# Kernel tuning notes

Hardware: AMD Instinct MI355X
Metric: run time of the kernel (lower is better)

## Reference

```python
import jax, jax.numpy as jnp
import numpy as np

L, D, DB, P, B = 33, 2048, 1024, 24, 2048
EPS = 1e-5

def _ln(x, g, b):
    # LayerNorm over last axis, eps matches torch default 1e-5
    mu = jnp.mean(x, axis=-1, keepdims=True)
    var = jnp.mean(jnp.square(x - mu), axis=-1, keepdims=True)
    return (x - mu) * jax.lax.rsqrt(var + EPS) * g + b

def setup_inputs() -> dict:
    key = jax.random.key(0)
    ks = jax.random.split(key, 8)
    s1 = 1.0 / np.sqrt(D)   # fan-in style scaling to keep activations sane
    s2 = 1.0 / np.sqrt(DB)
    sp = 1.0 / np.sqrt(P)
    return {
        "x":      jax.random.normal(ks[0], (B, L, D), jnp.float32),
        "pos_emb": jax.random.uniform(ks[1], (L, P), jnp.float32),
        "Wk":     jax.random.normal(ks[2], (P, D), jnp.float32) * sp,
        "W1":     jax.random.normal(ks[3], (L, D, DB), jnp.float32) * s1,
        "b1":     jnp.zeros((L, DB), jnp.float32),
        "ln1_g":  jnp.ones((L, DB), jnp.float32),
        "ln1_b":  jnp.zeros((L, DB), jnp.float32),
        "W2":     jax.random.normal(ks[4], (L, DB, D), jnp.float32) * s2,
        "b2":     jnp.zeros((L, D), jnp.float32),
        "ln2_g":  jnp.ones((L, D), jnp.float32),
        "ln2_b":  jnp.zeros((L, D), jnp.float32),
        "Wq1":    jax.random.normal(ks[5], (D, DB), jnp.float32) * s1,
        "bq1":    jnp.zeros((DB,), jnp.float32),
        "lnq_g":  jnp.ones((DB,), jnp.float32),
        "lnq_b":  jnp.zeros((DB,), jnp.float32),
        "Wq2":    jax.random.normal(ks[6], (DB, D), jnp.float32) * s2,
        "bq2":    jnp.zeros((D,), jnp.float32),
    }

def reference(x, pos_emb, Wk, W1, b1, ln1_g, ln1_b, W2, b2, ln2_g, ln2_b,
              Wq1, bq1, lnq_g, lnq_b, Wq2, bq2):
    # x: [B, L, D]
    z_L = x[:, -1, :]                                   # [B, D]
    keys = pos_emb @ Wk                                 # Eq.10: [L, D]
    # Eq.11 + Eq.4: per-layer value MLPs, grouped as batched GEMMs
    h = jax.nn.gelu(jnp.einsum('bld,ldk->blk', x, W1) + b1, approximate=False)
    h = _ln(h, ln1_g, ln1_b)                            # [B, L, DB]
    v = jnp.einsum('blk,lkd->bld', h, W2) + b2          # [B, L, D]
    values = _ln(v, ln2_g, ln2_b)                       # [B, L, D]
    # Eq.5: query from last layer
    hq = jax.nn.gelu(z_L @ Wq1 + bq1, approximate=False)
    hq = _ln(hq, lnq_g, lnq_b)
    q_tr = hq @ Wq2 + bq2                               # [B, D]
    query = 1.0 + jax.nn.elu(z_L + q_tr)                # [B, D]
    # Eq.7-9: single-query attention over depth + residual
    attn = jax.nn.softmax(query @ keys.T, axis=-1)      # [B, L]
    attended = jnp.einsum('bl,bld->bd', attn, values)   # [B, D]
    return z_L + attended
```

## Files before the change

kernel.cpp:

```cpp
#include <hip/hip_runtime.h>
#include <cstddef>
#include <cstdint>

#define Lc 33
#define Dc 2048
#define DBc 1024
#define Pc 24
#define Bc 2048

typedef __attribute__((ext_vector_type(4))) float f32x4;
typedef __attribute__((ext_vector_type(8))) short s16x8;
typedef __attribute__((ext_vector_type(4))) short s16x4;

__device__ __forceinline__ short bf16r(float f) {
  unsigned u = __float_as_uint(f);
  u = (u + 0x7fffu + ((u >> 16) & 1u)) >> 16;
  return (short)u;
}
__device__ __forceinline__ float bf2f(short s) {
  return __uint_as_float(((unsigned)(unsigned short)s) << 16);
}
__device__ __forceinline__ s16x8 pack8(const float* f) {
  s16x8 r;
#pragma unroll
  for (int i = 0; i < 8; ++i) r[i] = bf16r(f[i]);
  return r;
}
__device__ __forceinline__ void split8(const float* f, s16x8& hi, s16x8& lo) {
#pragma unroll
  for (int i = 0; i < 8; ++i) {
    short h = bf16r(f[i]);
    hi[i] = h;
    lo[i] = bf16r(f[i] - bf2f(h));
  }
}
__device__ __forceinline__ void gl_lds16(const void* g, void* l) {
  __builtin_amdgcn_global_load_lds(
      (const __attribute__((address_space(1))) unsigned int*)g,
      (__attribute__((address_space(3))) unsigned int*)l, 16, 0, 0);
}

#define BARw() __builtin_amdgcn_s_barrier()
#define VM4() asm volatile("s_waitcnt vmcnt(4)" ::: "memory")

__global__ __launch_bounds__(256)
void cvt_perm_kernel(const float* __restrict__ in,
                     unsigned short* __restrict__ outp) {
  const int row = blockIdx.x, z = blockIdx.y;
  const int k0 = threadIdx.x * 8;
  const float* src = in + ((size_t)row * Lc + z) * Dc + k0;
  f32x4 a = *(const f32x4*)(src);
  f32x4 b = *(const f32x4*)(src + 4);
  float f[8] = {a[0], a[1], a[2], a[3], b[0], b[1], b[2], b[3]};
  *(s16x8*)(outp + ((size_t)z * Bc + row) * Dc + k0) = pack8(f);
}

__global__ __launch_bounds__(256)
void keys_kernel(const float* __restrict__ pe, const float* __restrict__ Wk,
                 float* __restrict__ keys) {
  const int l = blockIdx.x;
  const int d = blockIdx.y * 256 + threadIdx.x;
  float s = 0.f;
#pragma unroll
  for (int p = 0; p < Pc; ++p) s += pe[l * Pc + p] * Wk[(size_t)p * Dc + d];
  keys[(size_t)l * Dc + d] = s;
}

template <int K, int N>
__global__ __launch_bounds__(256)
void transpose_w(const float* __restrict__ W, unsigned short* __restrict__ Wt) {
  const int z = blockIdx.z;
  const int k0 = blockIdx.x * 64, n0 = blockIdx.y * 64;
  __shared__ unsigned short tile[64][66];
  const int t = threadIdx.x;
  {
    const int r = t >> 2, cq = (t & 3) * 16;
    const float* src = W + (size_t)z * K * N + (size_t)(k0 + r) * N + n0 + cq;
#pragma unroll
    for (int i = 0; i < 16; i += 4) {
      f32x4 v = *(const f32x4*)(src + i);
#pragma unroll
      for (int j = 0; j < 4; ++j)
        tile[r][cq + i + j] = (unsigned short)bf16r(v[j]);
    }
  }
  __syncthreads();
  {
    const int n = t >> 2, kc = (t & 3) * 16;
    s16x8 o0, o1;
#pragma unroll
    for (int i = 0; i < 8; ++i) {
      o0[i] = tile[kc + i][n];
      o1[i] = tile[kc + 8 + i][n];
    }
    unsigned short* dst =
        Wt + (size_t)z * N * K + (size_t)(n0 + n) * K + k0 + kc;
    *(s16x8*)dst = o0;
    *(s16x8*)(dst + 8) = o1;
  }
}

__global__ __launch_bounds__(256)
void transpose_w2g(const float* __restrict__ W, const float* __restrict__ g,
                   const float* __restrict__ bvec, const float* __restrict__ b2,
                   unsigned short* __restrict__ Wt, float* __restrict__ gw,
                   float* __restrict__ bw) {
  constexpr int K = 1024, N = 2048;
  const int z = blockIdx.y;
  const int n0 = blockIdx.x * 64;
  __shared__ unsigned short tileG[64][66];
  __shared__ unsigned short tileW[64][66];
  const int t = threadIdx.x;
  const int rL = t >> 2, cq = (t & 3) * 16;
  const int nS = t >> 2, kc = (t & 3) * 16;
  float gwp = 0.f, bwp = 0.f;

  for (int kt = 0; kt < 16; ++kt) {
    {
      const float gs = g[(size_t)z * K + kt * 64 + rL];
      const float* src =
          W + (size_t)z * K * N + (size_t)(kt * 64 + rL) * N + n0 + cq;
#pragma unroll
      for (int i = 0; i < 16; i += 4) {
        f32x4 v = *(const f32x4*)(src + i);
#pragma unroll
        for (int j = 0; j < 4; ++j) {
          tileW[rL][cq + i + j] = (unsigned short)bf16r(v[j]);
          tileG[rL][cq + i + j] = (unsigned short)bf16r(gs * v[j]);
        }
      }
    }
    __syncthreads();
    {
      s16x8 o0, o1;
#pragma unroll
      for (int i = 0; i < 8; ++i) {
        o0[i] = tileG[kc + i][nS];
        o1[i] = tileG[kc + 8 + i][nS];
      }
#pragma unroll
      for (int i = 0; i < 16; ++i) {
        gwp += bf2f(tileG[kc + i][nS]);
        bwp += bvec[(size_t)z * K + kt * 64 + kc + i] * bf2f(tileW[kc + i][nS]);
      }
      unsigned short* dst =
          Wt + (size_t)z * N * K + (size_t)(n0 + nS) * K + kt * 64 + kc;
      *(s16x8*)dst = o0;
      *(s16x8*)(dst + 8) = o1;
    }
    __syncthreads();
  }
  gwp += __shfl_xor(gwp, 1);
  gwp += __shfl_xor(gwp, 2);
  bwp += __shfl_xor(bwp, 1);
  bwp += __shfl_xor(bwp, 2);
  if ((t & 3) == 0) {
    gw[(size_t)z * N + n0 + nS] = gwp;
    bw[(size_t)z * N + n0 + nS] = bwp + b2[(size_t)z * N + n0 + nS];
  }
}

template <int W>
__global__ __launch_bounds__(256)
void stats_w_kernel(const unsigned short* __restrict__ buf,
                    float* __restrict__ stats) {
  constexpr int E = W / 256;
  const int z = blockIdx.x;
  const int b = blockIdx.y;
  const int tid = threadIdx.x;
  const unsigned short* row = buf + ((size_t)z * Bc + b) * W;
  float s = 0.f, s2 = 0.f;
  if constexpr (E == 4) {
    s16x4 t = *(const s16x4*)(row + tid * 4);
#pragma unroll
    for (int i = 0; i < 4; ++i) {
      float v = bf2f(t[i]);
      s += v;
      s2 += v * v;
    }
  } else {
    s16x8 t = *(const s16x8*)(row + tid * 8);
#pragma unroll
    for (int i = 0; i < 8; ++i) {
      float v = bf2f(t[i]);
      s += v;
      s2 += v * v;
    }
  }
#pragma unroll
  for (int o = 32; o > 0; o >>= 1) {
    s += __shfl_xor(s, o);
    s2 += __shfl_xor(s2, o);
  }
  __shared__ float red[2][4];
  const int w = tid >> 6;
  if ((tid & 63) == 0) {
    red[0][w] = s;
    red[1][w] = s2;
  }
  __syncthreads();
  if (tid == 0) {
    stats[((size_t)z * Bc + b) * 2 + 0] =
        red[0][0] + red[0][1] + red[0][2] + red[0][3];
    stats[((size_t)z * Bc + b) * 2 + 1] =
        red[1][0] + red[1][1] + red[1][2] + red[1][3];
  }
}

template <int K, int N, int NBN, int GELU, int FUSE>
__global__ __launch_bounds__(512, 2)
void gemm8ph(const unsigned short* __restrict__ A,
             const unsigned short* __restrict__ Wt,
             const float* __restrict__ bias,
             unsigned short* __restrict__ outbuf,
             const float* __restrict__ gw, const float* __restrict__ bw,
             const float* __restrict__ stats1) {
  constexpr int NT = K / 64;
  constexpr int NIT = NT / 2;
  constexpr int NBM = 8;
  extern __shared__ __align__(16) char smem[];

  constexpr int nwg = 33 * NBM * NBN;
  constexpr int q = nwg >> 3, r = nwg & 7;
  const int orig = blockIdx.x;
  const int xcd = orig & 7;
  const int wgid =
      ((xcd < r) ? xcd * (q + 1) : r * (q + 1) + (xcd - r) * q) + (orig >> 3);
  const int z = wgid / (NBM * NBN);
  const int rem = wgid - z * (NBM * NBN);
  const int bm = rem / NBN, bn = rem - bm * NBN;

  const int tid = threadIdx.x, lane = tid & 63, wv = tid >> 6;
  const int wm = wv >> 2, wn = wv & 3;
  const int wr = wm * 128, wc = wn * 64;
  const int l15 = lane & 15, l4 = lane >> 4;

  f32x4 acc[8][4];
#pragma unroll
  for (int m = 0; m < 8; ++m)
#pragma unroll
    for (int n = 0; n < 4; ++n) {
      acc[m][n][0] = 0.f; acc[m][n][1] = 0.f;
      acc[m][n][2] = 0.f; acc[m][n][3] = 0.f;
    }

  const unsigned short* aRow[2];
  const unsigned short* bRow[2];
  {
    const unsigned short* Bbase = Wt + (size_t)z * N * K;
#pragma unroll
    for (int c = 0; c < 2; ++c) {
      const int rprime = wv * 16 + c * 8 + (lane >> 3);
      const int row = 2 * rprime + ((lane >> 2) & 1);
      const int chunk = (lane & 3) ^ (rprime & 3);
      aRow[c] = A + ((size_t)z * Bc + bm * 256 + row) * K + chunk * 8;
      bRow[c] = Bbase + (size_t)(bn * 256 + row) * K + chunk * 8;
    }
  }

  auto STAGE_A = [&](int t, int kh) {
    char* dst = smem + (t & 1) * 65536 + kh * 16384 + wv * 2048;
    const int ko = t * 64 + kh * 32;
#pragma unroll
    for (int c = 0; c < 2; ++c) gl_lds16(aRow[c] + ko, dst + c * 1024);
  };
  auto STAGE_B = [&](int t, int kh) {
    char* dst = smem + (t & 1) * 65536 + 32768 + kh * 16384 + wv * 2048;
    const int ko = t * 64 + kh * 32;
#pragma unroll
    for (int c = 0; c < 2; ++c) gl_lds16(bRow[c] + ko, dst + c * 1024);
  };
  s16x8 afr[4], bfr[4];
  auto LDA = [&](int d, int kh, int mh) {
#pragma unroll
    for (int m = 0; m < 4; ++m) {
      const int row = wr + (mh * 4 + m) * 16 + l15;
      const int rp = row >> 1;
      afr[m] = *(const s16x8*)(smem + d * 65536 + kh * 16384 + rp * 128 +
                               (row & 1) * 64 + ((l4 ^ (rp & 3)) << 4));
    }
  };
  auto LDB = [&](int d, int kh) {
#pragma unroll
    for (int n = 0; n < 4; ++n) {
      const int row = wc + n * 16 + l15;
      const int rp = row >> 1;
      bfr[n] = *(const s16x8*)(smem + d * 65536 + 32768 + kh * 16384 +
                               rp * 128 + (row & 1) * 64 +
                               ((l4 ^ (rp & 3)) << 4));
    }
  };

#define MFMA16(MH)                                                          \
  {                                                                         \
    __builtin_amdgcn_s_setprio(1);                                          \
    _Pragma("unroll") for (int m_ = 0; m_ < 4; ++m_) {                      \
      _Pragma("unroll") for (int n_ = 0; n_ < 4; ++n_) {                    \
        acc[(MH) * 4 + m_][n_] = __builtin_amdgcn_mfma_f32_16x16x32_bf16(   \
            afr[m_], bfr[n_], acc[(MH) * 4 + m_][n_], 0, 0, 0);             \
      }                                                                     \
    }                                                                       \
    __builtin_amdgcn_s_setprio(0);                                          \
  }

  STAGE_A(0, 0); STAGE_B(0, 0); STAGE_A(0, 1); STAGE_B(0, 1);
  STAGE_A(1, 0); STAGE_B(1, 0);
  VM4();
  BARw();

  for (int i = 0; i < NIT; ++i) {
    const int t0 = 2 * i, t1 = 2 * i + 1;
    LDA(0, 0, 0); LDB(0, 0);
    STAGE_A(t1, 1);
    BARw(); MFMA16(0); BARw();
    LDA(0, 0, 1);
    STAGE_B(t1, 1);
    BARw(); MFMA16(1); BARw();
    LDA(0, 1, 0); LDB(0, 1);
    if (t0 + 2 < NT) STAGE_A(t0 + 2, 0);
    BARw(); MFMA16(0); BARw();
    LDA(0, 1, 1);
    if (t0 + 2 < NT) STAGE_B(t0 + 2, 0);
    BARw(); MFMA16(1);
    VM4();
    BARw();
    LDA(1, 0, 0); LDB(1, 0);
    if (t0 + 2 < NT) STAGE_A(t0 + 2, 1);
    BARw(); MFMA16(0); BARw();
    LDA(1, 0, 1);
    if (t0 + 2 < NT) STAGE_B(t0 + 2, 1);
    BARw(); MFMA16(1); BARw();
    LDA(1, 1, 0); LDB(1, 1);
    if (t0 + 3 < NT) STAGE_A(t0 + 3, 0);
    BARw(); MFMA16(0); BARw();
    LDA(1, 1, 1);
    if (t0 + 3 < NT) STAGE_B(t0 + 3, 0);
    BARw(); MFMA16(1);
    VM4();
    BARw();
  }
#undef MFMA16

  float bsv[4], gwv[4], bwv[4];
#pragma unroll
  for (int n = 0; n < 4; ++n) {
    const int col = bn * 256 + wc + n * 16 + l15;
    if constexpr (FUSE) {
      gwv[n] = gw[(size_t)z * N + col];
      bwv[n] = bw[(size_t)z * N + col];
    } else {
      bsv[n] = bias[(size_t)z * N + col];
    }
  }

#pragma unroll
  for (int m = 0; m < 8; ++m) {
#pragma unroll
    for (int j = 0; j < 4; ++j) {
      const int grow = bm * 256 + wr + m * 16 + l4 * 4 + j;
      float mu = 0.f, rstd = 0.f;
      if constexpr (FUSE) {
        const float st0 = stats1[((size_t)z * Bc + grow) * 2 + 0];
        const float st1 = stats1[((size_t)z * Bc + grow) * 2 + 1];
        mu = st0 * (1.0f / K);
        const float var = st1 * (1.0f / K) - mu * mu;
        rstd = rsqrtf(var + 1e-5f);
      }
#pragma unroll
      for (int n = 0; n < 4; ++n) {
        const int col = bn * 256 + wc + n * 16 + l15;
        float v;
        if constexpr (FUSE) {
          v = rstd * acc[m][n][j] - (rstd * mu) * gwv[n] + bwv[n];
        } else {
          v = acc[m][n][j] + bsv[n];
        }
        if constexpr (GELU) v = 0.5f * v * (1.0f + erff(v * 0.70710678118f));
        outbuf[((size_t)z * Bc + grow) * N + col] = (unsigned short)bf16r(v);
      }
    }
  }
}

template <int MODE, int SPLITQ>
__global__ __launch_bounds__(256, 2)
void gemm_fused(const float* __restrict__ x,
                const unsigned short* __restrict__ hbuf,
                const float* __restrict__ hqF,
                const float* __restrict__ Wmain, const float* __restrict__ Wq,
                const float* __restrict__ bmain, const float* __restrict__ bq,
                unsigned short* __restrict__ outH, float* __restrict__ outHq,
                unsigned short* __restrict__ outV, float* __restrict__ outQ) {
  constexpr int K = (MODE == 1) ? 2048 : 1024;
  constexpr int N = (MODE == 1) ? 1024 : 2048;
  constexpr int BK = 32;
  constexpr int NT = K / BK;

  const int z = blockIdx.z;
  const int bm = blockIdx.x;
  const int bn = blockIdx.y;
  const int tid = threadIdx.x;
  const int lane = tid & 63;
  const int wid = tid >> 6;
  const int wr = (wid >> 1) * 64;
  const int wc = (wid & 1) * 64;
  const int l15 = lane & 15;
  const int kb = lane >> 4;

  const float* Bp = SPLITQ ? Wq : (Wmain + (size_t)z * K * N);

  __shared__ short Als[1 + SPLITQ][128][32];
  __shared__ short Bls[1 + SPLITQ][128][32];

  const f32x4 vzero = {0.f, 0.f, 0.f, 0.f};
  f32x4 acc[4][4];
#pragma unroll
  for (int m = 0; m < 4; ++m)
#pragma unroll
    for (int n = 0; n < 4; ++n) acc[m][n] = vzero;

  const int ar = tid >> 1;
  const int ak = (tid & 1) * 16;
  const int grow = bm * 128 + ar;

  const float* ApF = nullptr;
  const unsigned short* ApH = nullptr;
  if constexpr (MODE == 1) {
    const int lsel = SPLITQ ? (Lc - 1) : z;
    ApF = x + (size_t)grow * (Lc * Dc) + (size_t)lsel * Dc + ak;
  } else if constexpr (SPLITQ == 1) {
    ApF = hqF + (size_t)grow * DBc + ak;
  } else {
    ApH = hbuf + ((size_t)z * Bc + grow) * DBc + ak;
  }

  const int bnL = tid & 127;
  const int bj = tid >> 7;
  const int c0 = ((bnL >> 1) & 3) ^ bj;
  const int kc0 = c0 * 8;
  const int kc1 = (c0 ^ 2) * 8;
  const float* Bcol = Bp + (size_t)bn * 128 + bnL;

  float aF[16];
  s16x8 aH0, aH1;
  float bF[16];

  auto loadA = [&](int kt) {
    if constexpr (MODE == 2 && SPLITQ == 0) {
      const unsigned short* p = ApH + kt * BK;
      aH0 = *(const s16x8*)p;
      aH1 = *(const s16x8*)(p + 8);
    } else {
      const float* p = ApF + kt * BK;
#pragma unroll
      for (int i = 0; i < 4; ++i) {
        f32x4 t = *(const f32x4*)(p + i * 4);
#pragma unroll
        for (int j = 0; j < 4; ++j) aF[i * 4 + j] = t[j];
      }
    }
  };
  auto loadB = [&](int kt) {
    const float* p0 = Bcol + (size_t)(kt * BK + kc0) * N;
    const float* p1 = Bcol + (size_t)(kt * BK + kc1) * N;
#pragma unroll
    for (int i = 0; i < 8; ++i) bF[i] = p0[(size_t)i * N];
#pragma unroll
    for (int i = 0; i < 8; ++i) bF[8 + i] = p1[(size_t)i * N];
  };
  auto writeLDS = [&]() {
    if constexpr (MODE == 2 && SPLITQ == 0) {
      *(s16x8*)&Als[0][ar][ak] = aH0;
      *(s16x8*)&Als[0][ar][ak + 8] = aH1;
    } else if constexpr (SPLITQ == 0) {
      *(s16x8*)&Als[0][ar][ak] = pack8(aF);
      *(s16x8*)&Als[0][ar][ak + 8] = pack8(aF + 8);
    } else {
      s16x8 h0, l0, h1, l1;
      split8(aF, h0, l0);
      split8(aF + 8, h1, l1);
      *(s16x8*)&Als[0][ar][ak] = h0;
      *(s16x8*)&Als[1][ar][ak] = l0;
      *(s16x8*)&Als[0][ar][ak + 8] = h1;
      *(s16x8*)&Als[1][ar][ak + 8] = l1;
    }
    if constexpr (SPLITQ == 0) {
      *(s16x8*)&Bls[0][bnL][kc0] = pack8(bF);
      *(s16x8*)&Bls[0][bnL][kc1] = pack8(bF + 8);
    } else {
      s16x8 h0, l0, h1, l1;
      split8(bF, h0, l0);
      split8(bF + 8, h1, l1);
      *(s16x8*)&Bls[0][bnL][kc0] = h0;
      *(s16x8*)&Bls[1][bnL][kc0] = l0;
      *(s16x8*)&Bls[0][bnL][kc1] = h1;
      *(s16x8*)&Bls[1][bnL][kc1] = l1;
    }
  };

  loadA(0);
  loadB(0);
  for (int kt = 0; kt < NT; ++kt) {
    __syncthreads();
    writeLDS();
    if (kt + 1 < NT) {
      loadA(kt + 1);
      loadB(kt + 1);
    }
    __syncthreads();
    s16x8 af[4], bfv[4];
#pragma unroll
    for (int m = 0; m < 4; ++m)
      af[m] = *(const s16x8*)&Als[0][wr + m * 16 + l15][kb * 8];
#pragma unroll
    for (int n = 0; n < 4; ++n)
      bfv[n] = *(const s16x8*)&Bls[0][wc + n * 16 + l15][kb * 8];
    if constexpr (SPLITQ == 1) {
      s16x8 afl[4], bfl[4];
#pragma unroll
      for (int m = 0; m < 4; ++m)
        afl[m] = *(const s16x8*)&Als[1][wr + m * 16 + l15][kb * 8];
#pragma unroll
      for (int n = 0; n < 4; ++n)
        bfl[n] = *(const s16x8*)&Bls[1][wc + n * 16 + l15][kb * 8];
#pragma unroll
      for (int m = 0; m < 4; ++m)
#pragma unroll
        for (int n = 0; n < 4; ++n) {
          acc[m][n] = __builtin_amdgcn_mfma_f32_16x16x32_bf16(
              af[m], bfv[n], acc[m][n], 0, 0, 0);
          acc[m][n] = __builtin_amdgcn_mfma_f32_16x16x32_bf16(
              af[m], bfl[n], acc[m][n], 0, 0, 0);
          acc[m][n] = __builtin_amdgcn_mfma_f32_16x16x32_bf16(
              afl[m], bfv[n], acc[m][n], 0, 0, 0);
        }
    } else {
#pragma unroll
      for (int m = 0; m < 4; ++m)
#pragma unroll
        for (int n = 0; n < 4; ++n)
          acc[m][n] = __builtin_amdgcn_mfma_f32_16x16x32_bf16(
              af[m], bfv[n], acc[m][n], 0, 0, 0);
    }
  }

  const float* biasP = SPLITQ ? bq : (bmain + (size_t)z * N);
#pragma unroll
  for (int m = 0; m < 4; ++m) {
    const int r0 = bm * 128 + wr + m * 16 + kb * 4;
#pragma unroll
    for (int n = 0; n < 4; ++n) {
      const int col = bn * 128 + wc + n * 16 + l15;
      const float bs = biasP[col];
#pragma unroll
      for (int j = 0; j < 4; ++j) {
        const int r = r0 + j;
        const float v = acc[m][n][j] + bs;
        if constexpr (MODE == 1 && SPLITQ == 0) {
          const float g = 0.5f * v * (1.0f + erff(v * 0.70710678118f));
          outH[((size_t)z * Bc + r) * DBc + col] = (unsigned short)bf16r(g);
        } else if constexpr (MODE == 1 && SPLITQ == 1) {
          const float g = 0.5f * v * (1.0f + erff(v * 0.70710678118f));
          outHq[(size_t)r * DBc + col] = g;
        } else if constexpr (MODE == 2 && SPLITQ == 0) {
          outV[((size_t)z * Bc + r) * Dc + col] = (unsigned short)bf16r(v);
        } else {
          const float zl =
              x[(size_t)r * (Lc * Dc) + (size_t)(Lc - 1) * Dc + col];
          const float t = zl + v;
          outQ[(size_t)r * Dc + col] = (t > 0.f) ? (1.f + t) : __expf(t);
        }
      }
    }
  }
}

template <int W>
__global__ __launch_bounds__(256)
void ln_kernel(unsigned short* __restrict__ buf, const float* __restrict__ gmain,
               const float* __restrict__ bmain) {
  constexpr int E = W / 256;
  const int z = blockIdx.x;
  const int b = blockIdx.y;
  const int tid = threadIdx.x;
  unsigned short* row = buf + ((size_t)z * Bc + b) * W;
  float v[E];
  if constexpr (E == 4) {
    s16x4 t = *(const s16x4*)(row + tid * 4);
#pragma unroll
    for (int i = 0; i < 4; ++i) v[i] = bf2f(t[i]);
  } else {
    s16x8 t = *(const s16x8*)(row + tid * 8);
#pragma unroll
    for (int i = 0; i < 8; ++i) v[i] = bf2f(t[i]);
  }
  float s = 0.f, s2 = 0.f;
#pragma unroll
  for (int i = 0; i < E; ++i) {
    s += v[i];
    s2 += v[i] * v[i];
  }
#pragma unroll
  for (int o = 32; o > 0; o >>= 1) {
    s += __shfl_xor(s, o);
    s2 += __shfl_xor(s2, o);
  }
  __shared__ float red[2][4];
  const int w = tid >> 6;
  if ((tid & 63) == 0) {
    red[0][w] = s;
    red[1][w] = s2;
  }
  __syncthreads();
  s = red[0][0] + red[0][1] + red[0][2] + red[0][3];
  s2 = red[1][0] + red[1][1] + red[1][2] + red[1][3];
  const float mu = s * (1.0f / W);
  const float var = s2 * (1.0f / W) - mu * mu;
  const float rstd = rsqrtf(var + 1e-5f);
  const float* G = gmain + (size_t)z * W;
  const float* Bt = bmain + (size_t)z * W;
  if constexpr (E == 4) {
    f32x4 gv = *(const f32x4*)(G + tid * 4);
    f32x4 bv = *(const f32x4*)(Bt + tid * 4);
    s16x4 o;
#pragma unroll
    for (int i = 0; i < 4; ++i)
      o[i] = bf16r((v[i] - mu) * rstd * gv[i] + bv[i]);
    *(s16x4*)(row + tid * 4) = o;
  } else {
    f32x4 g0 = *(const f32x4*)(G + tid * 8);
    f32x4 g1 = *(const f32x4*)(G + tid * 8 + 4);
    f32x4 b0 = *(const f32x4*)(Bt + tid * 8);
    f32x4 b1 = *(const f32x4*)(Bt + tid * 8 + 4);
    s16x8 o;
#pragma unroll
    for (int i = 0; i < 4; ++i) {
      o[i] = bf16r((v[i] - mu) * rstd * g0[i] + b0[i]);
      o[i + 4] = bf16r((v[i + 4] - mu) * rstd * g1[i] + b1[i]);
    }
    *(s16x8*)(row + tid * 8) = o;
  }
}

__global__ __launch_bounds__(256)
void ln_f32_kernel(float* __restrict__ buf, const float* __restrict__ g,
                   const float* __restrict__ bb) {
  const int r = blockIdx.x;
  const int tid = threadIdx.x;
  float* row = buf + (size_t)r * DBc;
  f32x4 v = *(const f32x4*)(row + tid * 4);
  float s = 0.f, s2 = 0.f;
#pragma unroll
  for (int i = 0; i < 4; ++i) {
    s += v[i];
    s2 += v[i] * v[i];
  }
#pragma unroll
  for (int o = 32; o > 0; o >>= 1) {
    s += __shfl_xor(s, o);
    s2 += __shfl_xor(s2, o);
  }
  __shared__ float red[2][4];
  const int w = tid >> 6;
  if ((tid & 63) == 0) {
    red[0][w] = s;
    red[1][w] = s2;
  }
  __syncthreads();
  s = red[0][0] + red[0][1] + red[0][2] + red[0][3];
  s2 = red[1][0] + red[1][1] + red[1][2] + red[1][3];
  const float mu = s * (1.0f / DBc);
  const float var = s2 * (1.0f / DBc) - mu * mu;
  const float rstd = rsqrtf(var + 1e-5f);
  f32x4 gv = *(const f32x4*)(g + tid * 4);
  f32x4 bv = *(const f32x4*)(bb + tid * 4);
  f32x4 o;
#pragma unroll
  for (int i = 0; i < 4; ++i) o[i] = (v[i] - mu) * rstd * gv[i] + bv[i];
  *(f32x4*)(row + tid * 4) = o;
}

__global__ __launch_bounds__(256)
void attn_kernel(const float* __restrict__ x, const float* __restrict__ query,
                 const float* __restrict__ keys,
                 const unsigned short* __restrict__ vals,
                 const float* __restrict__ stats, const float* __restrict__ g2,
                 const float* __restrict__ b2ln, float* __restrict__ out) {
  const int b = blockIdx.x;
  const int tid = threadIdx.x;
  const int d0 = tid * 8;

  float qv[8];
  {
    f32x4 t0 = *(const f32x4*)(query + (size_t)b * Dc + d0);
    f32x4 t1 = *(const f32x4*)(query + (size_t)b * Dc + d0 + 4);
#pragma unroll
    for (int i = 0; i < 4; ++i) {
      qv[i] = t0[i];
      qv[i + 4] = t1[i];
    }
  }
  float s[33];
#pragma unroll
  for (int l = 0; l < 33; ++l) {
    const float* kp = keys + (size_t)l * Dc + d0;
    f32x4 k0 = *(const f32x4*)kp;
    f32x4 k1 = *(const f32x4*)(kp + 4);
    float t = 0.f;
#pragma unroll
    for (int i = 0; i < 4; ++i) t += qv[i] * k0[i] + qv[i + 4] * k1[i];
    s[l] = t;
  }
#pragma unroll
  for (int l = 0; l < 33; ++l) {
    float v = s[l];
#pragma unroll
    for (int o = 32; o > 0; o >>= 1) v += __shfl_xor(v, o);
    s[l] = v;
  }
  __shared__ float sred[4][33];
  __shared__ float sl[33];
  const int w = tid >> 6;
  if ((tid & 63) == 0) {
#pragma unroll
    for (int l = 0; l < 33; ++l) sred[w][l] = s[l];
  }
  __syncthreads();
  if (tid < 33)
    sl[tid] = sred[0][tid] + sred[1][tid] + sred[2][tid] + sred[3][tid];
  __syncthreads();

  float m = -1e30f;
#pragma unroll
  for (int l = 0; l < 33; ++l) m = fmaxf(m, sl[l]);
  float p[33];
  float sum = 0.f;
#pragma unroll
  for (int l = 0; l < 33; ++l) {
    p[l] = __expf(sl[l] - m);
    sum += p[l];
  }
  const float inv = 1.0f / sum;

  float acc8[8];
  {
    const float* zl = x + (size_t)b * (Lc * Dc) + (size_t)(Lc - 1) * Dc + d0;
    f32x4 z0 = *(const f32x4*)zl;
    f32x4 z1 = *(const f32x4*)(zl + 4);
#pragma unroll
    for (int i = 0; i < 4; ++i) {
      acc8[i] = z0[i];
      acc8[i + 4] = z1[i];
    }
  }
#pragma unroll
  for (int l = 0; l < 33; ++l) {
    const float st0 = stats[((size_t)l * Bc + b) * 2 + 0];
    const float st1 = stats[((size_t)l * Bc + b) * 2 + 1];
    const float mu = st0 * (1.0f / Dc);
    const float var = st1 * (1.0f / Dc) - mu * mu;
    const float rstd = rsqrtf(var + 1e-5f);
    const float a = p[l] * inv;
    s16x8 vv = *(const s16x8*)(vals + ((size_t)l * Bc + b) * Dc + d0);
    const float* gp = g2 + (size_t)l * Dc + d0;
    const float* bp = b2ln + (size_t)l * Dc + d0;
    f32x4 g0 = *(const f32x4*)gp, g1 = *(const f32x4*)(gp + 4);
    f32x4 b0 = *(const f32x4*)bp, b1 = *(const f32x4*)(bp + 4);
#pragma unroll
    for (int i = 0; i < 4; ++i) {
      acc8[i] += a * ((bf2f(vv[i]) - mu) * rstd * g0[i] + b0[i]);
      acc8[i + 4] += a * ((bf2f(vv[i + 4]) - mu) * rstd * g1[i] + b1[i]);
    }
  }
  f32x4 o0, o1;
#pragma unroll
  for (int i = 0; i < 4; ++i) {
    o0[i] = acc8[i];
    o1[i] = acc8[i + 4];
  }
  *(f32x4*)(out + (size_t)b * Dc + d0) = o0;
  *(f32x4*)(out + (size_t)b * Dc + d0 + 4) = o1;
}

extern "C" void kernel_launch(void* const* d_in, const int* in_sizes, int n_in,
                              void* d_out, int out_size, void* d_ws,
                              size_t ws_size, hipStream_t stream) {
  const float* x = (const float*)d_in[0];
  const float* pe = (const float*)d_in[1];
  const float* Wk = (const float*)d_in[2];
  const float* W1 = (const float*)d_in[3];
  const float* b1 = (const float*)d_in[4];
  const float* ln1g = (const float*)d_in[5];
  const float* ln1b = (const float*)d_in[6];
  const float* W2 = (const float*)d_in[7];
  const float* b2 = (const float*)d_in[8];
  const float* ln2g = (const float*)d_in[9];
  const float* ln2b = (const float*)d_in[10];
  const float* Wq1 = (const float*)d_in[11];
  const float* bq1 = (const float*)d_in[12];
  const float* lnqg = (const float*)d_in[13];
  const float* lnqb = (const float*)d_in[14];
  const float* Wq2 = (const float*)d_in[15];
  const float* bq2 = (const float*)d_in[16];
  float* out = (float*)d_out;
  char* ws = (char*)d_ws;

  float* keysP = (float*)(ws);
  float* queryP = (float*)(ws + 270336);
  float* hqP = (float*)(ws + 17047552);
  float* stats1P = (float*)(ws + 25436160);
  float* stats2P = (float*)(ws + 25976832);
  float* gwP = (float*)(ws + 26517504);
  float* bwP = (float*)(ws + 26787840);
  unsigned short* hP = (unsigned short*)(ws + 27058176);
  unsigned short* xbfP = (unsigned short*)(ws + 165470208);
  unsigned short* valsP = (unsigned short*)(ws + 165470208);
  unsigned short* W1tP = (unsigned short*)(ws + 442294272);
  unsigned short* W2gtP = (unsigned short*)(ws + 442294272);

  const bool fast = (ws_size >= 580706304ull);
  bool use8 = fast;
  if (fast) {
    if (hipFuncSetAttribute(
            reinterpret_cast<const void*>(&gemm8ph<2048, 1024, 4, 1, 0>),
            hipFuncAttributeMaxDynamicSharedMemorySize, 131072) != hipSuccess)
      use8 = false;
    if (hipFuncSetAttribute(
            reinterpret_cast<const void*>(&gemm8ph<1024, 2048, 8, 0, 1>),
            hipFuncAttributeMaxDynamicSharedMemorySize, 131072) != hipSuccess)
      use8 = false;
  }

  keys_kernel<<<dim3(33, 8), 256, 0, stream>>>(pe, Wk, keysP);

  gemm_fused<1, 1><<<dim3(16, 8, 1), 256, 0, stream>>>(
      x, nullptr, nullptr, nullptr, Wq1, nullptr, bq1, nullptr, hqP, nullptr,
      nullptr);

  if (use8) {
    cvt_perm_kernel<<<dim3(2048, 33), 256, 0, stream>>>(x, xbfP);
    transpose_w<2048, 1024><<<dim3(32, 16, 33), 256, 0, stream>>>(W1, W1tP);
    gemm8ph<2048, 1024, 4, 1, 0>
        <<<dim3(33 * 8 * 4), 512, 131072, stream>>>(xbfP, W1tP, b1, hP,
                                                    nullptr, nullptr, nullptr);
    stats_w_kernel<1024><<<dim3(33, 2048), 256, 0, stream>>>(hP, stats1P);
    ln_f32_kernel<<<dim3(2048), 256, 0, stream>>>(hqP, lnqg, lnqb);
    transpose_w2g<<<dim3(32, 33), 256, 0, stream>>>(W2, ln1g, ln1b, b2, W2gtP,
                                                    gwP, bwP);
    gemm8ph<1024, 2048, 8, 0, 1>
        <<<dim3(33 * 8 * 8), 512, 131072, stream>>>(hP, W2gtP, nullptr, valsP,
                                                    gwP, bwP, stats1P);
    stats_w_kernel<2048><<<dim3(33, 2048), 256, 0, stream>>>(valsP, stats2P);
  } else {
    gemm_fused<1, 0><<<dim3(16, 8, 33), 256, 0, stream>>>(
        x, nullptr, nullptr, W1, nullptr, b1, nullptr, hP, nullptr, nullptr,
        nullptr);
    ln_kernel<1024><<<dim3(33, 2048), 256, 0, stream>>>(hP, ln1g, ln1b);
    ln_f32_kernel<<<dim3(2048), 256, 0, stream>>>(hqP, lnqg, lnqb);
    gemm_fused<2, 0><<<dim3(16, 16, 33), 256, 0, stream>>>(
        x, hP, nullptr, W2, nullptr, b2, nullptr, nullptr, nullptr, valsP,
        nullptr);
    stats_w_kernel<2048><<<dim3(33, 2048), 256, 0, stream>>>(valsP, stats2P);
  }

  gemm_fused<2, 1><<<dim3(16, 16, 1), 256, 0, stream>>>(
      x, nullptr, hqP, nullptr, Wq2, nullptr, bq2, nullptr, nullptr, nullptr,
      queryP);

  attn_kernel<<<dim3(2048), 256, 0, stream>>>(x, queryP, keysP, valsP,
                                              stats2P, ln2g, ln2b, out);
}
```

Baseline: 1.529 ms.

## Fuse value LayerNorm stats into attention and split-bf16 MFMA query GEMMs

Drops the separate pass that computed per-row LayerNorm statistics over the value tensor. The attention kernel now computes each row's mean and variance in the same loop that forms the query-key scores. The query-path GEMMs (Wq1 and Wq2) move to a new double-buffered kernel fed through global-to-LDS loads. It emulates fp32 precision with hi/lo bf16 splits and three MFMAs per tile, using pre-split, transposed operands prepared by new helper kernels. The new query path needs a larger workspace and is enabled only when the workspace is big enough. The attention kernel now reads the value rows twice.

```diff
diff --git a/kernel.cpp b/kernel.cpp
--- a/kernel.cpp
+++ b/kernel.cpp
@@ -42,6 +42,7 @@
 
 #define BARw() __builtin_amdgcn_s_barrier()
 #define VM4() asm volatile("s_waitcnt vmcnt(4)" ::: "memory")
+#define VM0() asm volatile("s_waitcnt vmcnt(0)" ::: "memory")
 
 __global__ __launch_bounds__(256)
 void cvt_perm_kernel(const float* __restrict__ in,
@@ -56,6 +57,22 @@
 }
 
 __global__ __launch_bounds__(256)
+void cvt_split_z_kernel(const float* __restrict__ x,
+                        unsigned short* __restrict__ zhi,
+                        unsigned short* __restrict__ zlo) {
+  const int row = blockIdx.x;
+  const int k0 = threadIdx.x * 8;
+  const float* src = x + ((size_t)row * Lc + (Lc - 1)) * Dc + k0;
+  f32x4 a = *(const f32x4*)(src);
+  f32x4 b = *(const f32x4*)(src + 4);
+  float f[8] = {a[0], a[1], a[2], a[3], b[0], b[1], b[2], b[3]};
+  s16x8 h, l;
+  split8(f, h, l);
+  *(s16x8*)(zhi + (size_t)row * Dc + k0) = h;
+  *(s16x8*)(zlo + (size_t)row * Dc + k0) = l;
+}
+
+__global__ __launch_bounds__(256)
 void keys_kernel(const float* __restrict__ pe, const float* __restrict__ Wk,
                  float* __restrict__ keys) {
   const int l = blockIdx.x;
@@ -97,6 +114,48 @@
         Wt + (size_t)z * N * K + (size_t)(n0 + n) * K + k0 + kc;
     *(s16x8*)dst = o0;
     *(s16x8*)(dst + 8) = o1;
+  }
+}
+
+template <int K, int N>
+__global__ __launch_bounds__(256)
+void transpose_w_split(const float* __restrict__ W,
+                       unsigned short* __restrict__ Whi,
+                       unsigned short* __restrict__ Wlo) {
+  const int k0 = blockIdx.x * 64, n0 = blockIdx.y * 64;
+  __shared__ unsigned short th[64][66];
+  __shared__ unsigned short tl[64][66];
+  const int t = threadIdx.x;
+  {
+    const int r = t >> 2, cq = (t & 3) * 16;
+    const float* src = W + (size_t)(k0 + r) * N + n0 + cq;
+#pragma unroll
+    for (int i = 0; i < 16; i += 4) {
+      f32x4 v = *(const f32x4*)(src + i);
+#pragma unroll
+      for (int j = 0; j < 4; ++j) {
+        short h = bf16r(v[j]);
+        th[r][cq + i + j] = (unsigned short)h;
+        tl[r][cq + i + j] = (unsigned short)bf16r(v[j] - bf2f(h));
+      }
+    }
+  }
+  __syncthreads();
+  {
+    const int n = t >> 2, kc = (t & 3) * 16;
+    s16x8 h0, h1, l0, l1;
+#pragma unroll
+    for (int i = 0; i < 8; ++i) {
+      h0[i] = th[kc + i][n];
+      h1[i] = th[kc + 8 + i][n];
+      l0[i] = tl[kc + i][n];
+      l1[i] = tl[kc + 8 + i][n];
+    }
+    size_t o = (size_t)(n0 + n) * K + k0 + kc;
+    *(s16x8*)(Whi + o) = h0;
+    *(s16x8*)(Whi + o + 8) = h1;
+    *(s16x8*)(Wlo + o) = l0;
+    *(s16x8*)(Wlo + o + 8) = l1;
   }
 }
 
@@ -382,6 +441,114 @@
   }
 }
 
+template <int K, int N, int MODE>
+__global__ __launch_bounds__(256, 2)
+void gemm2ph_split(const unsigned short* __restrict__ Ahi,
+                   const unsigned short* __restrict__ Alo,
+                   const unsigned short* __restrict__ Bhi,
+                   const unsigned short* __restrict__ Blo,
+                   const float* __restrict__ bias, const float* __restrict__ x,
+                   float* __restrict__ outF) {
+  constexpr int NT = K / 32;
+  const int bm = blockIdx.x, bn = blockIdx.y;
+  const int tid = threadIdx.x, lane = tid & 63, w = tid >> 6;
+  const int wr = (w >> 1) * 64, wc = (w & 1) * 64;
+  const int l15 = lane & 15, l4 = lane >> 4;
+
+  __shared__ __align__(16) unsigned short LS[2][4][128 * 32];
+
+  f32x4 acc[4][4];
+#pragma unroll
+  for (int m = 0; m < 4; ++m)
+#pragma unroll
+    for (int n = 0; n < 4; ++n) {
+      acc[m][n][0] = 0.f; acc[m][n][1] = 0.f;
+      acc[m][n][2] = 0.f; acc[m][n][3] = 0.f;
+    }
+
+  const unsigned short* srcA[2][2];
+  const unsigned short* srcB[2][2];
+#pragma unroll
+  for (int j = 0; j < 2; ++j) {
+    const int idx = j * 256 + tid;
+    const int row = idx >> 2;
+    const int ch = (idx & 3) ^ (row & 3);
+    srcA[0][j] = Ahi + (size_t)(bm * 128 + row) * K + ch * 8;
+    srcA[1][j] = Alo + (size_t)(bm * 128 + row) * K + ch * 8;
+    srcB[0][j] = Bhi + (size_t)(bn * 128 + row) * K + ch * 8;
+    srcB[1][j] = Blo + (size_t)(bn * 128 + row) * K + ch * 8;
+  }
+
+  auto stage = [&](int buf, int kt) {
+    const int ko = kt * 32;
+#pragma unroll
+    for (int j = 0; j < 2; ++j) {
+      gl_lds16(srcA[0][j] + ko, (char*)&LS[buf][0][0] + j * 4096 + w * 1024);
+      gl_lds16(srcA[1][j] + ko, (char*)&LS[buf][1][0] + j * 4096 + w * 1024);
+      gl_lds16(srcB[0][j] + ko, (char*)&LS[buf][2][0] + j * 4096 + w * 1024);
+      gl_lds16(srcB[1][j] + ko, (char*)&LS[buf][3][0] + j * 4096 + w * 1024);
+    }
+  };
+
+  stage(0, 0);
+  VM0();
+  BARw();
+
+  for (int kt = 0; kt < NT; ++kt) {
+    const int cur = kt & 1;
+    if (kt + 1 < NT) stage(cur ^ 1, kt + 1);
+    s16x8 ah[4], al[4], bh[4], bl[4];
+#pragma unroll
+    for (int m = 0; m < 4; ++m) {
+      const int row = wr + m * 16 + l15;
+      const int off = row * 64 + ((l4 ^ (row & 3)) << 4);
+      ah[m] = *(const s16x8*)((const char*)&LS[cur][0][0] + off);
+      al[m] = *(const s16x8*)((const char*)&LS[cur][1][0] + off);
+    }
+#pragma unroll
+    for (int n = 0; n < 4; ++n) {
+      const int row = wc + n * 16 + l15;
+      const int off = row * 64 + ((l4 ^ (row & 3)) << 4);
+      bh[n] = *(const s16x8*)((const char*)&LS[cur][2][0] + off);
+      bl[n] = *(const s16x8*)((const char*)&LS[cur][3][0] + off);
+    }
+#pragma unroll
+    for (int m = 0; m < 4; ++m)
+#pragma unroll
+      for (int n = 0; n < 4; ++n) {
+        acc[m][n] = __builtin_amdgcn_mfma_f32_16x16x32_bf16(al[m], bh[n],
+                                                            acc[m][n], 0, 0, 0);
+        acc[m][n] = __builtin_amdgcn_mfma_f32_16x16x32_bf16(ah[m], bl[n],
+                                                            acc[m][n], 0, 0, 0);
+        acc[m][n] = __builtin_amdgcn_mfma_f32_16x16x32_bf16(ah[m], bh[n],
+                                                            acc[m][n], 0, 0, 0);
+      }
+    VM0();
+    BARw();
+  }
+
+#pragma unroll
+  for (int m = 0; m < 4; ++m) {
+#pragma unroll
+    for (int j = 0; j < 4; ++j) {
+      const int r = bm * 128 + wr + m * 16 + l4 * 4 + j;
+#pragma unroll
+      for (int n = 0; n < 4; ++n) {
+        const int col = bn * 128 + wc + n * 16 + l15;
+        float v = acc[m][n][j] + bias[col];
+        if constexpr (MODE == 1) {
+          v = 0.5f * v * (1.0f + erff(v * 0.70710678118f));
+          outF[(size_t)r * N + col] = v;
+        } else {
+          const float zl = x[((size_t)r * Lc + (Lc - 1)) * Dc + col];
+          const float t = zl + v;
+          outF[(size_t)r * N + col] = (t > 0.f) ? (1.f + t) : __expf(t);
+        }
+      }
+    }
+  }
+}
+
 template <int MODE, int SPLITQ>
 __global__ __launch_bounds__(256, 2)
 void gemm_fused(const float* __restrict__ x,
@@ -681,14 +848,62 @@
 }
 
 __global__ __launch_bounds__(256)
+void ln_f32_split_kernel(const float* __restrict__ buf,
+                         const float* __restrict__ g,
+                         const float* __restrict__ bb,
+                         unsigned short* __restrict__ hqhi,
+                         unsigned short* __restrict__ hqlo) {
+  const int r = blockIdx.x;
+  const int tid = threadIdx.x;
+  const float* row = buf + (size_t)r * DBc;
+  f32x4 v = *(const f32x4*)(row + tid * 4);
+  float s = 0.f, s2 = 0.f;
+#pragma unroll
+  for (int i = 0; i < 4; ++i) {
+    s += v[i];
+    s2 += v[i] * v[i];
+  }
+#pragma unroll
+  for (int o = 32; o > 0; o >>= 1) {
+    s += __shfl_xor(s, o);
+    s2 += __shfl_xor(s2, o);
+  }
+  __shared__ float red[2][4];
+  const int w = tid >> 6;
+  if ((tid & 63) == 0) {
+    red[0][w] = s;
+    red[1][w] = s2;
+  }
+  __syncthreads();
+  s = red[0][0] + red[0][1] + red[0][2] + red[0][3];
+  s2 = red[1][0] + red[1][1] + red[1][2] + red[1][3];
+  const float mu = s * (1.0f / DBc);
+  const float var = s2 * (1.0f / DBc) - mu * mu;
+  const float rstd = rsqrtf(var + 1e-5f);
+  f32x4 gv = *(const f32x4*)(g + tid * 4);
+  f32x4 bv = *(const f32x4*)(bb + tid * 4);
+  s16x4 oh, ol;
+#pragma unroll
+  for (int i = 0; i < 4; ++i) {
+    const float o = (v[i] - mu) * rstd * gv[i] + bv[i];
+    short h = bf16r(o);
+    oh[i] = h;
+    ol[i] = bf16r(o - bf2f(h));
+  }
+  *(s16x4*)(hqhi + (size_t)r * DBc + tid * 4) = oh;
+  *(s16x4*)(hqlo + (size_t)r * DBc + tid * 4) = ol;
+}
+
+__global__ __launch_bounds__(256)
 void attn_kernel(const float* __restrict__ x, const float* __restrict__ query,
                  const float* __restrict__ keys,
                  const unsigned short* __restrict__ vals,
-                 const float* __restrict__ stats, const float* __restrict__ g2,
-                 const float* __restrict__ b2ln, float* __restrict__ out) {
+                 const float* __restrict__ g2, const float* __restrict__ b2ln,
+                 float* __restrict__ out) {
   const int b = blockIdx.x;
   const int tid = threadIdx.x;
   const int d0 = tid * 8;
+  const int w = tid >> 6;
 
   float qv[8];
   {
@@ -700,44 +915,58 @@
       qv[i + 4] = t1[i];
     }
   }
-  float s[33];
+
+  __shared__ float red[4][33][3];
+  __shared__ float fin[33][3];
+
 #pragma unroll
   for (int l = 0; l < 33; ++l) {
+    s16x8 vv = *(const s16x8*)(vals + ((size_t)l * Bc + b) * Dc + d0);
     const float* kp = keys + (size_t)l * Dc + d0;
     f32x4 k0 = *(const f32x4*)kp;
     f32x4 k1 = *(const f32x4*)(kp + 4);
-    float t = 0.f;
-#pragma unroll
-    for (int i = 0; i < 4; ++i) t += qv[i] * k0[i] + qv[i + 4] * k1[i];
-    s[l] = t;
-  }
-#pragma unroll
-  for (int l = 0; l < 33; ++l) {
-    float v = s[l];
-#pragma unroll
-    for (int o = 32; o > 0; o >>= 1) v += __shfl_xor(v, o);
-    s[l] = v;
-  }
-  __shared__ float sred[4][33];
-  __shared__ float sl[33];
-  const int w = tid >> 6;
-  if ((tid & 63) == 0) {
-#pragma unroll
-    for (int l = 0; l < 33; ++l) sred[w][l] = s[l];
+    float t = 0.f, s = 0.f, s2 = 0.f;
+#pragma unroll
+    for (int i = 0; i < 4; ++i) {
+      t += qv[i] * k0[i] + qv[i + 4] * k1[i];
+      float va = bf2f(vv[i]), vb = bf2f(vv[i + 4]);
+      s += va + vb;
+      s2 += va * va + vb * vb;
+    }
+#pragma unroll
+    for (int o = 32; o > 0; o >>= 1) {
+      t += __shfl_xor(t, o);
+      s += __shfl_xor(s, o);
+      s2 += __shfl_xor(s2, o);
+    }
+    if ((tid & 63) == 0) {
+      red[w][l][0] = t;
+      red[w][l][1] = s;
+      red[w][l][2] = s2;
+    }
   }
   __syncthreads();
-  if (tid < 33)
-    sl[tid] = sred[0][tid] + sred[1][tid] + sred[2][tid] + sred[3][tid];
+  if (tid < 33) {
+    float t = red[0][tid][0] + red[1][tid][0] + red[2][tid][0] + red[3][tid][0];
+    float s = red[0][tid][1] + red[1][tid][1] + red[2][tid][1] + red[3][tid][1];
+    float s2 =
+        red[0][tid][2] + red[1][tid][2] + red[2][tid][2] + red[3][tid][2];
+    const float mu = s * (1.0f / Dc);
+    const float var = s2 * (1.0f / Dc) - mu * mu;
+    fin[tid][0] = t;
+    fin[tid][1] = mu;
+    fin[tid][2] = rsqrtf(var + 1e-5f);
+  }
   __syncthreads();
 
   float m = -1e30f;
 #pragma unroll
-  for (int l = 0; l < 33; ++l) m = fmaxf(m, sl[l]);
+  for (int l = 0; l < 33; ++l) m = fmaxf(m, fin[l][0]);
   float p[33];
   float sum = 0.f;
 #pragma unroll
   for (int l = 0; l < 33; ++l) {
-    p[l] = __expf(sl[l] - m);
+    p[l] = __expf(fin[l][0] - m);
     sum += p[l];
   }
   const float inv = 1.0f / sum;
@@ -755,11 +984,8 @@
   }
 #pragma unroll
   for (int l = 0; l < 33; ++l) {
-    const float st0 = stats[((size_t)l * Bc + b) * 2 + 0];
-    const float st1 = stats[((size_t)l * Bc + b) * 2 + 1];
-    const float mu = st0 * (1.0f / Dc);
-    const float var = st1 * (1.0f / Dc) - mu * mu;
-    const float rstd = rsqrtf(var + 1e-5f);
+    const float mu = fin[l][1];
+    const float rstd = fin[l][2];
     const float a = p[l] * inv;
     s16x8 vv = *(const s16x8*)(vals + ((size_t)l * Bc + b) * Dc + d0);
     const float* gp = g2 + (size_t)l * Dc + d0;
@@ -807,9 +1033,10 @@
 
   float* keysP = (float*)(ws);
   float* queryP = (float*)(ws + 270336);
+  unsigned short* zhiP = (unsigned short*)(ws + 270336);
+  unsigned short* zloP = (unsigned short*)(ws + 270336 + 8388608);
   float* hqP = (float*)(ws + 17047552);
   float* stats1P = (float*)(ws + 25436160);
-  float* stats2P = (float*)(ws + 25976832);
   float* gwP = (float*)(ws + 26517504);
   float* bwP = (float*)(ws + 26787840);
   unsigned short* hP = (unsigned short*)(ws + 27058176);
@@ -817,8 +1044,15 @@
   unsigned short* valsP = (unsigned short*)(ws + 165470208);
   unsigned short* W1tP = (unsigned short*)(ws + 442294272);
   unsigned short* W2gtP = (unsigned short*)(ws + 442294272);
+  unsigned short* hqHiP = (unsigned short*)(ws + 442294272);
+  unsigned short* hqLoP = (unsigned short*)(ws + 446488576);
+  unsigned short* Wq1tHiP = (unsigned short*)(ws + 580706304);
+  unsigned short* Wq1tLoP = (unsigned short*)(ws + 584900608);
+  unsigned short* Wq2tHiP = (unsigned short*)(ws + 589094912);
+  unsigned short* Wq2tLoP = (unsigned short*)(ws + 593289216);
 
   const bool fast = (ws_size >= 580706304ull);
+  const bool fastq = (ws_size >= 597483520ull);
   bool use8 = fast;
   if (fast) {
     if (hipFuncSetAttribute(
@@ -830,12 +1064,21 @@
             hipFuncAttributeMaxDynamicSharedMemorySize, 131072) != hipSuccess)
       use8 = false;
   }
+  const bool useq = use8 && fastq;
 
   keys_kernel<<<dim3(33, 8), 256, 0, stream>>>(pe, Wk, keysP);
 
-  gemm_fused<1, 1><<<dim3(16, 8, 1), 256, 0, stream>>>(
-      x, nullptr, nullptr, nullptr, Wq1, nullptr, bq1, nullptr, hqP, nullptr,
-      nullptr);
+  if (useq) {
+    cvt_split_z_kernel<<<dim3(2048), 256, 0, stream>>>(x, zhiP, zloP);
+    transpose_w_split<2048, 1024><<<dim3(32, 16), 256, 0, stream>>>(
+        Wq1, Wq1tHiP, Wq1tLoP);
+    gemm2ph_split<2048, 1024, 1><<<dim3(16, 8), 256, 0, stream>>>(
+        zhiP, zloP, Wq1tHiP, Wq1tLoP, bq1, nullptr, hqP);
+  } else {
+    gemm_fused<1, 1><<<dim3(16, 8, 1), 256, 0, stream>>>(
+        x, nullptr, nullptr, nullptr, Wq1, nullptr, bq1, nullptr, hqP, nullptr,
+        nullptr);
+  }
 
   if (use8) {
     cvt_perm_kernel<<<dim3(2048, 33), 256, 0, stream>>>(x, xbfP);
@@ -844,13 +1087,26 @@
         <<<dim3(33 * 8 * 4), 512, 131072, stream>>>(xbfP, W1tP, b1, hP,
                                                     nullptr, nullptr, nullptr);
     stats_w_kernel<1024><<<dim3(33, 2048), 256, 0, stream>>>(hP, stats1P);
-    ln_f32_kernel<<<dim3(2048), 256, 0, stream>>>(hqP, lnqg, lnqb);
+
+    if (useq) {
+      ln_f32_split_kernel<<<dim3(2048), 256, 0, stream>>>(hqP, lnqg, lnqb,
+                                                          hqHiP, hqLoP);
+      transpose_w_split<1024, 2048><<<dim3(16, 32), 256, 0, stream>>>(
+          Wq2, Wq2tHiP, Wq2tLoP);
+      gemm2ph_split<1024, 2048, 2><<<dim3(16, 16), 256, 0, stream>>>(
+          hqHiP, hqLoP, Wq2tHiP, Wq2tLoP, bq2, x, queryP);
+    } else {
+      ln_f32_kernel<<<dim3(2048), 256, 0, stream>>>(hqP, lnqg, lnqb);
+      gemm_fused<2, 1><<<dim3(16, 16, 1), 256, 0, stream>>>(
+          x, nullptr, hqP, nullptr, Wq2, nullptr, bq2, nullptr, nullptr,
+          nullptr, queryP);
+    }
+
     transpose_w2g<<<dim3(32, 33), 256, 0, stream>>>(W2, ln1g, ln1b, b2, W2gtP,
                                                     gwP, bwP);
     gemm8ph<1024, 2048, 8, 0, 1>
         <<<dim3(33 * 8 * 8), 512, 131072, stream>>>(hP, W2gtP, nullptr, valsP,
                                                     gwP, bwP, stats1P);
-    stats_w_kernel<2048><<<dim3(33, 2048), 256, 0, stream>>>(valsP, stats2P);
   } else {
     gemm_fused<1, 0><<<dim3(16, 8, 33), 256, 0, stream>>>(
         x, nullptr, nullptr, W1, nullptr, b1, nullptr, hP, nullptr, nullptr,
@@ -860,13 +1116,11 @@
     gemm_fused<2, 0><<<dim3(16, 16, 33), 256, 0, stream>>>(
         x, hP, nullptr, W2, nullptr, b2, nullptr, nullptr, nullptr, valsP,
         nullptr);
-    stats_w_kernel<2048><<<dim3(33, 2048), 256, 0, stream>>>(valsP, stats2P);
-  }
-
-  gemm_fused<2, 1><<<dim3(16, 16, 1), 256, 0, stream>>>(
-      x, nullptr, hqP, nullptr, Wq2, nullptr, bq2, nullptr, nullptr, nullptr,
-      queryP);
-
-  attn_kernel<<<dim3(2048), 256, 0, stream>>>(x, queryP, keysP, valsP,
-                                              stats2P, ln2g, ln2b, out);
-}
+    gemm_fused<2, 1><<<dim3(16, 16, 1), 256, 0, stream>>>(
+        x, nullptr, hqP, nullptr, Wq2, nullptr, bq2, nullptr, nullptr, nullptr,
+        queryP);
+  }
+
+  attn_kernel<<<dim3(2048), 256, 0, stream>>>(x, queryP, keysP, valsP, ln2g,
+                                              ln2b, out);
+}
```

Result: slower. 1.594 ms (+4.2%).
